# Optimization experiments

Hardware: AMD Instinct MI355X
Metric: run time of the kernel (lower is better)

The kernel has to match this reference:

```python
import jax, jax.numpy as jnp
import numpy as np

TEMPERATURE = 0.2
HYPER_GAMMA = 0.5
EPS = 1e-12  # torch F.normalize / cosine_similarity eps guard (1e-12 / 1e-8)

def setup_inputs() -> dict:
    key = jax.random.key(0)
    k1, k2 = jax.random.split(key)
    B, D = 4096, 1024
    return {
        "emb_i": jax.random.normal(k1, (B, D), dtype=jnp.float32),
        "emb_j": jax.random.normal(k2, (B, D), dtype=jnp.float32),
    }

def _l2_normalize(x, eps=EPS):
    n = jnp.sqrt(jnp.sum(x * x, axis=1, keepdims=True))
    return x / jnp.maximum(n, eps)

def reference(emb_i, emb_j):
    B = emb_i.shape[0]
    z_i = _l2_normalize(emb_i)
    z_j = _l2_normalize(emb_j)
    # cosine similarity of unit vectors == dot product; sim[a, b] = <z_j[a], z_i[b]>
    sim = jnp.einsum('ad,bd->ab', z_j, z_i)  # [B, B]
    sim_positive = jnp.diagonal(sim)
    positives_exp = jnp.exp(-sim_positive + TEMPERATURE)
    neg_mask = 1.0 - jnp.eye(B, dtype=sim.dtype)
    negatives_exp = neg_mask * jnp.exp(sim - TEMPERATURE)
    positives_sum = jnp.sum(jnp.log1p(positives_exp)) / B
    negatives_sum = jnp.sum(jnp.log1p(negatives_exp)) / (B * (B - 1))
    return HYPER_GAMMA * positives_sum + (1.0 - HYPER_GAMMA) * negatives_sum
```

## Files before the change

### kernel.cpp

```cpp
#include <hip/hip_runtime.h>
#include <math.h>

#define B_ROWS 4096
#define D_DIM  1024
static constexpr float TEMP = 0.2f;

typedef __attribute__((ext_vector_type(8))) short bf16x8;
typedef __attribute__((ext_vector_type(4))) float f32x4;

__device__ inline unsigned short f2bf(float f) {
    unsigned int u = __float_as_uint(f);
    u += 0x7fffu + ((u >> 16) & 1u);
    return (unsigned short)(u >> 16);
}

__device__ inline void gload_lds16(const unsigned short* g, unsigned short* l) {
    __builtin_amdgcn_global_load_lds(
        (const __attribute__((address_space(1))) unsigned int*)g,
        (__attribute__((address_space(3))) unsigned int*)l,
        16, 0, 0);
}


__global__ __launch_bounds__(256) void norm_cast_kernel(
        const float* __restrict__ emb_i, const float* __restrict__ emb_j,
        unsigned short* __restrict__ Zi, unsigned short* __restrict__ Zj,
        float* __restrict__ w) {
    const int tid = threadIdx.x;
    if (blockIdx.x == 0 && tid == 0) {
        w[0] = 0.0f; w[1] = 0.0f;
        ((unsigned int*)w)[2] = 0u;
    }
    const int wave = tid >> 6, lane = tid & 63;
    const int row = blockIdx.x * 4 + wave;
    const float* src; unsigned short* dst; int r;
    if (row < B_ROWS) { src = emb_i; dst = Zi; r = row; }
    else              { src = emb_j; dst = Zj; r = row - B_ROWS; }

    const float4* p = (const float4*)(src + (size_t)r * D_DIM);
    float4 v0 = p[lane], v1 = p[64 + lane], v2 = p[128 + lane], v3 = p[192 + lane];
    float s = v0.x*v0.x + v0.y*v0.y + v0.z*v0.z + v0.w*v0.w
            + v1.x*v1.x + v1.y*v1.y + v1.z*v1.z + v1.w*v1.w
            + v2.x*v2.x + v2.y*v2.y + v2.z*v2.z + v2.w*v2.w
            + v3.x*v3.x + v3.y*v3.y + v3.z*v3.z + v3.w*v3.w;
    #pragma unroll
    for (int m = 1; m < 64; m <<= 1) s += __shfl_xor(s, m, 64);
    const float inv = 1.0f / fmaxf(sqrtf(s), 1e-12f);

    ushort4* q = (ushort4*)(dst + (size_t)r * D_DIM);
    ushort4 o0 = { f2bf(v0.x*inv), f2bf(v0.y*inv), f2bf(v0.z*inv), f2bf(v0.w*inv) };
    ushort4 o1 = { f2bf(v1.x*inv), f2bf(v1.y*inv), f2bf(v1.z*inv), f2bf(v1.w*inv) };
    ushort4 o2 = { f2bf(v2.x*inv), f2bf(v2.y*inv), f2bf(v2.z*inv), f2bf(v2.w*inv) };
    ushort4 o3 = { f2bf(v3.x*inv), f2bf(v3.y*inv), f2bf(v3.z*inv), f2bf(v3.w*inv) };
    q[lane] = o0; q[64 + lane] = o1; q[128 + lane] = o2; q[192 + lane] = o3;
}

__global__ __launch_bounds__(256, 2) void simloss_mfma_kernel(
        const unsigned short* __restrict__ Zi,
        const unsigned short* __restrict__ Zj,
        float* __restrict__ w, float* __restrict__ out) {
    __shared__ __align__(16) unsigned short lA[128 * 32];
    __shared__ __align__(16) unsigned short lB[256 * 32];
    __shared__ float rn[4], rp[4];

    const int tid  = threadIdx.x;
    const int lane = tid & 63;
    const int wave = tid >> 6;
    const int wy = wave >> 1, wx = wave & 1;
    const int rowBase = blockIdx.y * 128;
    const int colBase = blockIdx.x * 256;

    const int lrow = lane >> 2;
    const int lp   = lane & 3;
    const int lc   = (lp - (lrow >> 1)) & 3;
    const unsigned short* gA0 = Zj + (size_t)(rowBase + (2*wave+0)*16 + lrow) * D_DIM + lc*8;
    const unsigned short* gA1 = Zj + (size_t)(rowBase + (2*wave+1)*16 + lrow) * D_DIM + lc*8;
    const unsigned short* gB0 = Zi + (size_t)(colBase + (4*wave+0)*16 + lrow) * D_DIM + lc*8;
    const unsigned short* gB1 = Zi + (size_t)(colBase + (4*wave+1)*16 + lrow) * D_DIM + lc*8;
    const unsigned short* gB2 = Zi + (size_t)(colBase + (4*wave+2)*16 + lrow) * D_DIM + lc*8;
    const unsigned short* gB3 = Zi + (size_t)(colBase + (4*wave+3)*16 + lrow) * D_DIM + lc*8;
    unsigned short* sA0 = lA + (2*wave+0) * 512;
    unsigned short* sA1 = lA + (2*wave+1) * 512;
    unsigned short* sB0 = lB + (4*wave+0) * 512;
    unsigned short* sB1 = lB + (4*wave+1) * 512;
    unsigned short* sB2 = lB + (4*wave+2) * 512;
    unsigned short* sB3 = lB + (4*wave+3) * 512;

    const int fr = lane & 15;
    const int q4 = lane >> 4;
    const int p0 = (q4 + (fr >> 1)) & 3;
    const unsigned short* fA = lA + (wy * 64 + fr) * 32 + p0 * 8;
    const unsigned short* fB = lB + (wx * 128 + fr) * 32 + p0 * 8;

    f32x4 acc[4][8];
    #pragma unroll
    for (int i = 0; i < 4; ++i)
        #pragma unroll
        for (int j = 0; j < 8; ++j)
            acc[i][j] = (f32x4){0.f, 0.f, 0.f, 0.f};

    for (int k0 = 0; k0 < D_DIM; k0 += 32) {
        __syncthreads();
        gload_lds16(gA0, sA0); gload_lds16(gA1, sA1);
        gload_lds16(gB0, sB0); gload_lds16(gB1, sB1);
        gload_lds16(gB2, sB2); gload_lds16(gB3, sB3);
        gA0 += 32; gA1 += 32; gB0 += 32; gB1 += 32; gB2 += 32; gB3 += 32;
        __syncthreads();

        bf16x8 a[4], b[8];
        #pragma unroll
        for (int i = 0; i < 4; ++i) a[i] = *(const bf16x8*)(fA + i * 16 * 32);
        #pragma unroll
        for (int j = 0; j < 8; ++j) b[j] = *(const bf16x8*)(fB + j * 16 * 32);
        #pragma unroll
        for (int i = 0; i < 4; ++i)
            #pragma unroll
            for (int j = 0; j < 8; ++j)
                acc[i][j] = __builtin_amdgcn_mfma_f32_16x16x32_bf16(
                    a[i], b[j], acc[i][j], 0, 0, 0);
    }

    const int cr = q4 * 4;
    const int cc = lane & 15;
    float neg = 0.f, pos = 0.f;
    #pragma unroll
    for (int i = 0; i < 4; ++i) {
        const int abase = rowBase + wy * 64 + i * 16 + cr;
        #pragma unroll
        for (int j = 0; j < 8; ++j) {
            const int b = colBase + wx * 128 + j * 16 + cc;
            #pragma unroll
            for (int r = 0; r < 4; ++r) {
                const float x = acc[i][j][r] - TEMP;
                if (abase + r == b) pos += __logf(1.0f + __expf(-x));
                else                neg += __logf(1.0f + __expf(x));
            }
        }
    }
    #pragma unroll
    for (int off = 32; off > 0; off >>= 1) {
        neg += __shfl_down(neg, off, 64);
        pos += __shfl_down(pos, off, 64);
    }
    if (lane == 0) { rn[wave] = neg; rp[wave] = pos; }
    __syncthreads();
    if (tid == 0) {
        atomicAdd(&w[1], rn[0] + rn[1] + rn[2] + rn[3]);
        if ((int)blockIdx.x == (int)(blockIdx.y >> 1))
            atomicAdd(&w[0], rp[0] + rp[1] + rp[2] + rp[3]);
        __threadfence();
        unsigned int done = atomicAdd(((unsigned int*)w) + 2, 1u);
        if (done == gridDim.x * gridDim.y - 1) {
            const float psum = atomicAdd(&w[0], 0.0f);
            const float nsum = atomicAdd(&w[1], 0.0f);
            out[0] = 0.5f * (psum / (float)B_ROWS)
                   + 0.5f * (nsum / ((float)B_ROWS * (float)(B_ROWS - 1)));
        }
    }
}

extern "C" void kernel_launch(void* const* d_in, const int* in_sizes, int n_in,
                              void* d_out, int out_size, void* d_ws, size_t ws_size,
                              hipStream_t stream) {
    const float* emb_i = (const float*)d_in[0];
    const float* emb_j = (const float*)d_in[1];
    float* w = (float*)d_ws;
    unsigned short* Zi = (unsigned short*)(w + 16);
    unsigned short* Zj = Zi + (size_t)B_ROWS * D_DIM;
    float* out = (float*)d_out;

    norm_cast_kernel<<<2 * B_ROWS / 4, 256, 0, stream>>>(emb_i, emb_j, Zi, Zj, w);
    dim3 grid(B_ROWS / 256, B_ROWS / 128);
    simloss_mfma_kernel<<<grid, 256, 0, stream>>>(Zi, Zj, w, out);
}
```

Baseline: 125.9 us.

## Fuse normalize-cast into GEMM kernel with grid-wide spin barrier

```diff
diff --git a/kernel.cpp b/kernel.cpp
--- a/kernel.cpp
+++ b/kernel.cpp
@@ -22,43 +22,15 @@
 }
 
 
-__global__ __launch_bounds__(256) void norm_cast_kernel(
-        const float* __restrict__ emb_i, const float* __restrict__ emb_j,
-        unsigned short* __restrict__ Zi, unsigned short* __restrict__ Zj,
-        float* __restrict__ w) {
-    const int tid = threadIdx.x;
-    if (blockIdx.x == 0 && tid == 0) {
-        w[0] = 0.0f; w[1] = 0.0f;
-        ((unsigned int*)w)[2] = 0u;
-    }
-    const int wave = tid >> 6, lane = tid & 63;
-    const int row = blockIdx.x * 4 + wave;
-    const float* src; unsigned short* dst; int r;
-    if (row < B_ROWS) { src = emb_i; dst = Zi; r = row; }
-    else              { src = emb_j; dst = Zj; r = row - B_ROWS; }
-
-    const float4* p = (const float4*)(src + (size_t)r * D_DIM);
-    float4 v0 = p[lane], v1 = p[64 + lane], v2 = p[128 + lane], v3 = p[192 + lane];
-    float s = v0.x*v0.x + v0.y*v0.y + v0.z*v0.z + v0.w*v0.w
-            + v1.x*v1.x + v1.y*v1.y + v1.z*v1.z + v1.w*v1.w
-            + v2.x*v2.x + v2.y*v2.y + v2.z*v2.z + v2.w*v2.w
-            + v3.x*v3.x + v3.y*v3.y + v3.z*v3.z + v3.w*v3.w;
-    #pragma unroll
-    for (int m = 1; m < 64; m <<= 1) s += __shfl_xor(s, m, 64);
-    const float inv = 1.0f / fmaxf(sqrtf(s), 1e-12f);
-
-    ushort4* q = (ushort4*)(dst + (size_t)r * D_DIM);
-    ushort4 o0 = { f2bf(v0.x*inv), f2bf(v0.y*inv), f2bf(v0.z*inv), f2bf(v0.w*inv) };
-    ushort4 o1 = { f2bf(v1.x*inv), f2bf(v1.y*inv), f2bf(v1.z*inv), f2bf(v1.w*inv) };
-    ushort4 o2 = { f2bf(v2.x*inv), f2bf(v2.y*inv), f2bf(v2.z*inv), f2bf(v2.w*inv) };
-    ushort4 o3 = { f2bf(v3.x*inv), f2bf(v3.y*inv), f2bf(v3.z*inv), f2bf(v3.w*inv) };
-    q[lane] = o0; q[64 + lane] = o1; q[128 + lane] = o2; q[192 + lane] = o3;
+__global__ void init_ctrl_kernel(float* __restrict__ w) {
+    if (threadIdx.x < 2) w[threadIdx.x] = 0.0f;
+    else if (threadIdx.x < 4) ((unsigned int*)w)[threadIdx.x] = 0u;
 }
 
-__global__ __launch_bounds__(256, 2) void simloss_mfma_kernel(
-        const unsigned short* __restrict__ Zi,
-        const unsigned short* __restrict__ Zj,
-        float* __restrict__ w, float* __restrict__ out) {
+__global__ __launch_bounds__(256, 2) void fused_simloss_kernel(
+        const float* __restrict__ emb_i, const float* __restrict__ emb_j,
+        unsigned short* Zi, unsigned short* Zj,
+        float* w, float* out) {
     __shared__ __align__(16) unsigned short lA[128 * 32];
     __shared__ __align__(16) unsigned short lB[256 * 32];
     __shared__ float rn[4], rp[4];
@@ -66,6 +38,45 @@
     const int tid  = threadIdx.x;
     const int lane = tid & 63;
     const int wave = tid >> 6;
+    const int bid  = blockIdx.y * gridDim.x + blockIdx.x;
+    const unsigned int nblk = gridDim.x * gridDim.y;
+
+    #pragma unroll
+    for (int it = 0; it < 4; ++it) {
+        const int row = bid * 16 + it * 4 + wave;
+        const float* src; unsigned short* dst; int r;
+        if (row < B_ROWS) { src = emb_i; dst = Zi; r = row; }
+        else              { src = emb_j; dst = Zj; r = row - B_ROWS; }
+
+        const float4* p = (const float4*)(src + (size_t)r * D_DIM);
+        float4 v0 = p[lane], v1 = p[64 + lane], v2 = p[128 + lane], v3 = p[192 + lane];
+        float s = v0.x*v0.x + v0.y*v0.y + v0.z*v0.z + v0.w*v0.w
+                + v1.x*v1.x + v1.y*v1.y + v1.z*v1.z + v1.w*v1.w
+                + v2.x*v2.x + v2.y*v2.y + v2.z*v2.z + v2.w*v2.w
+                + v3.x*v3.x + v3.y*v3.y + v3.z*v3.z + v3.w*v3.w;
+        #pragma unroll
+        for (int m = 1; m < 64; m <<= 1) s += __shfl_xor(s, m, 64);
+        const float inv = 1.0f / fmaxf(sqrtf(s), 1e-12f);
+
+        ushort4* q = (ushort4*)(dst + (size_t)r * D_DIM);
+        ushort4 o0 = { f2bf(v0.x*inv), f2bf(v0.y*inv), f2bf(v0.z*inv), f2bf(v0.w*inv) };
+        ushort4 o1 = { f2bf(v1.x*inv), f2bf(v1.y*inv), f2bf(v1.z*inv), f2bf(v1.w*inv) };
+        ushort4 o2 = { f2bf(v2.x*inv), f2bf(v2.y*inv), f2bf(v2.z*inv), f2bf(v2.w*inv) };
+        ushort4 o3 = { f2bf(v3.x*inv), f2bf(v3.y*inv), f2bf(v3.z*inv), f2bf(v3.w*inv) };
+        q[lane] = o0; q[64 + lane] = o1; q[128 + lane] = o2; q[192 + lane] = o3;
+    }
+
+    __syncthreads();
+    unsigned int* ctr = (unsigned int*)w + 2;
+    if (tid == 0) {
+        __threadfence();
+        __hip_atomic_fetch_add(ctr, 1u, __ATOMIC_RELEASE, __HIP_MEMORY_SCOPE_AGENT);
+        while (__hip_atomic_load(ctr, __ATOMIC_ACQUIRE, __HIP_MEMORY_SCOPE_AGENT) < nblk)
+            __builtin_amdgcn_s_sleep(8);
+        __threadfence();
+    }
+    __syncthreads();
+
     const int wy = wave >> 1, wx = wave & 1;
     const int rowBase = blockIdx.y * 128;
     const int colBase = blockIdx.x * 256;
@@ -149,8 +160,8 @@
         if ((int)blockIdx.x == (int)(blockIdx.y >> 1))
             atomicAdd(&w[0], rp[0] + rp[1] + rp[2] + rp[3]);
         __threadfence();
-        unsigned int done = atomicAdd(((unsigned int*)w) + 2, 1u);
-        if (done == gridDim.x * gridDim.y - 1) {
+        unsigned int done = atomicAdd(((unsigned int*)w) + 3, 1u);
+        if (done == nblk - 1) {
             const float psum = atomicAdd(&w[0], 0.0f);
             const float nsum = atomicAdd(&w[1], 0.0f);
             out[0] = 0.5f * (psum / (float)B_ROWS)
@@ -169,7 +180,7 @@
     unsigned short* Zj = Zi + (size_t)B_ROWS * D_DIM;
     float* out = (float*)d_out;
 
-    norm_cast_kernel<<<2 * B_ROWS / 4, 256, 0, stream>>>(emb_i, emb_j, Zi, Zj, w);
+    init_ctrl_kernel<<<1, 64, 0, stream>>>(w);
     dim3 grid(B_ROWS / 256, B_ROWS / 128);
-    simloss_mfma_kernel<<<grid, 256, 0, stream>>>(Zi, Zj, w, out);
+    fused_simloss_kernel<<<grid, 256, 0, stream>>>(emb_i, emb_j, Zi, Zj, w, out);
 }
```

Measured after the change: 195.7 us. +55.5%, slower.

## Switch similarity GEMM from bf16 to scaled fp8 e4m3 MFMA

Applied to the files above, without the earlier changes.

```diff
diff --git a/kernel.cpp b/kernel.cpp
--- a/kernel.cpp
+++ b/kernel.cpp
@@ -4,17 +4,39 @@
 #define B_ROWS 4096
 #define D_DIM  1024
 static constexpr float TEMP = 0.2f;
-
-typedef __attribute__((ext_vector_type(8))) short bf16x8;
+static constexpr float FP8_SCALE = 16.0f;
+static constexpr float INV_S2 = 1.0f / 256.0f;
+
 typedef __attribute__((ext_vector_type(4))) float f32x4;
 
-__device__ inline unsigned short f2bf(float f) {
+__device__ inline unsigned char f2fp8(float f) {
     unsigned int u = __float_as_uint(f);
-    u += 0x7fffu + ((u >> 16) & 1u);
-    return (unsigned short)(u >> 16);
-}
-
-__device__ inline void gload_lds16(const unsigned short* g, unsigned short* l) {
+    unsigned int s = (u >> 24) & 0x80u;
+    float af = fabsf(f);
+    unsigned char b;
+    if (af >= 0x1.0p-6f) {
+        unsigned int au = u & 0x7fffffffu;
+        unsigned int lsb = (au >> 20) & 1u;
+        au += 0x7ffffu + lsb;
+        int e = (int)(au >> 23) - 127 + 7;
+        unsigned int m = (au >> 20) & 7u;
+        if (e > 15 || (e == 15 && m > 6)) b = 0x7e;
+        else b = (unsigned char)((e << 3) | m);
+    } else {
+        int q = (int)rintf(af * 512.0f);
+        b = (unsigned char)(q >= 8 ? 0x08 : q);
+    }
+    return (unsigned char)(b | s);
+}
+
+__device__ inline unsigned int f2fp8x4(float4 v) {
+    return (unsigned int)f2fp8(v.x)
+         | ((unsigned int)f2fp8(v.y) << 8)
+         | ((unsigned int)f2fp8(v.z) << 16)
+         | ((unsigned int)f2fp8(v.w) << 24);
+}
+
+__device__ inline void gload_lds16(const unsigned char* g, unsigned char* l) {
     __builtin_amdgcn_global_load_lds(
         (const __attribute__((address_space(1))) unsigned int*)g,
         (__attribute__((address_space(3))) unsigned int*)l,
@@ -24,7 +46,7 @@
 
 __global__ __launch_bounds__(256) void norm_cast_kernel(
         const float* __restrict__ emb_i, const float* __restrict__ emb_j,
-        unsigned short* __restrict__ Zi, unsigned short* __restrict__ Zj,
+        unsigned char* __restrict__ Zi8, unsigned char* __restrict__ Zj8,
         float* __restrict__ w) {
     const int tid = threadIdx.x;
     if (blockIdx.x == 0 && tid == 0) {
@@ -33,9 +55,9 @@
     }
     const int wave = tid >> 6, lane = tid & 63;
     const int row = blockIdx.x * 4 + wave;
-    const float* src; unsigned short* dst; int r;
-    if (row < B_ROWS) { src = emb_i; dst = Zi; r = row; }
-    else              { src = emb_j; dst = Zj; r = row - B_ROWS; }
+    const float* src; unsigned char* dst; int r;
+    if (row < B_ROWS) { src = emb_i; dst = Zi8; r = row; }
+    else              { src = emb_j; dst = Zj8; r = row - B_ROWS; }
 
     const float4* p = (const float4*)(src + (size_t)r * D_DIM);
     float4 v0 = p[lane], v1 = p[64 + lane], v2 = p[128 + lane], v3 = p[192 + lane];
@@ -45,22 +67,25 @@
             + v3.x*v3.x + v3.y*v3.y + v3.z*v3.z + v3.w*v3.w;
     #pragma unroll
     for (int m = 1; m < 64; m <<= 1) s += __shfl_xor(s, m, 64);
-    const float inv = 1.0f / fmaxf(sqrtf(s), 1e-12f);
-
-    ushort4* q = (ushort4*)(dst + (size_t)r * D_DIM);
-    ushort4 o0 = { f2bf(v0.x*inv), f2bf(v0.y*inv), f2bf(v0.z*inv), f2bf(v0.w*inv) };
-    ushort4 o1 = { f2bf(v1.x*inv), f2bf(v1.y*inv), f2bf(v1.z*inv), f2bf(v1.w*inv) };
-    ushort4 o2 = { f2bf(v2.x*inv), f2bf(v2.y*inv), f2bf(v2.z*inv), f2bf(v2.w*inv) };
-    ushort4 o3 = { f2bf(v3.x*inv), f2bf(v3.y*inv), f2bf(v3.z*inv), f2bf(v3.w*inv) };
-    q[lane] = o0; q[64 + lane] = o1; q[128 + lane] = o2; q[192 + lane] = o3;
-}
-
-__global__ __launch_bounds__(256, 2) void simloss_mfma_kernel(
-        const unsigned short* __restrict__ Zi,
-        const unsigned short* __restrict__ Zj,
+    const float inv = FP8_SCALE / fmaxf(sqrtf(s), 1e-12f);
+
+    float4 a0 = {v0.x*inv, v0.y*inv, v0.z*inv, v0.w*inv};
+    float4 a1 = {v1.x*inv, v1.y*inv, v1.z*inv, v1.w*inv};
+    float4 a2 = {v2.x*inv, v2.y*inv, v2.z*inv, v2.w*inv};
+    float4 a3 = {v3.x*inv, v3.y*inv, v3.z*inv, v3.w*inv};
+    unsigned int* q = (unsigned int*)(dst + (size_t)r * D_DIM);
+    q[lane]       = f2fp8x4(a0);
+    q[64 + lane]  = f2fp8x4(a1);
+    q[128 + lane] = f2fp8x4(a2);
+    q[192 + lane] = f2fp8x4(a3);
+}
+
+__global__ __launch_bounds__(256, 2) void simloss_mfma_fp8_kernel(
+        const unsigned char* __restrict__ Zi8,
+        const unsigned char* __restrict__ Zj8,
         float* __restrict__ w, float* __restrict__ out) {
-    __shared__ __align__(16) unsigned short lA[128 * 32];
-    __shared__ __align__(16) unsigned short lB[256 * 32];
+    __shared__ __align__(16) unsigned char lA[128 * 64];
+    __shared__ __align__(16) unsigned char lB[256 * 64];
     __shared__ float rn[4], rp[4];
 
     const int tid  = threadIdx.x;
@@ -72,25 +97,29 @@
 
     const int lrow = lane >> 2;
     const int lp   = lane & 3;
-    const int lc   = (lp - (lrow >> 1)) & 3;
-    const unsigned short* gA0 = Zj + (size_t)(rowBase + (2*wave+0)*16 + lrow) * D_DIM + lc*8;
-    const unsigned short* gA1 = Zj + (size_t)(rowBase + (2*wave+1)*16 + lrow) * D_DIM + lc*8;
-    const unsigned short* gB0 = Zi + (size_t)(colBase + (4*wave+0)*16 + lrow) * D_DIM + lc*8;
-    const unsigned short* gB1 = Zi + (size_t)(colBase + (4*wave+1)*16 + lrow) * D_DIM + lc*8;
-    const unsigned short* gB2 = Zi + (size_t)(colBase + (4*wave+2)*16 + lrow) * D_DIM + lc*8;
-    const unsigned short* gB3 = Zi + (size_t)(colBase + (4*wave+3)*16 + lrow) * D_DIM + lc*8;
-    unsigned short* sA0 = lA + (2*wave+0) * 512;
-    unsigned short* sA1 = lA + (2*wave+1) * 512;
-    unsigned short* sB0 = lB + (4*wave+0) * 512;
-    unsigned short* sB1 = lB + (4*wave+1) * 512;
-    unsigned short* sB2 = lB + (4*wave+2) * 512;
-    unsigned short* sB3 = lB + (4*wave+3) * 512;
+    const int lc   = (lp - (lrow >> 2)) & 3;
+    const unsigned char* gA0 = Zj8 + (size_t)(rowBase + (2*wave+0)*16 + lrow) * D_DIM + lc*16;
+    const unsigned char* gA1 = Zj8 + (size_t)(rowBase + (2*wave+1)*16 + lrow) * D_DIM + lc*16;
+    const unsigned char* gB0 = Zi8 + (size_t)(colBase + (4*wave+0)*16 + lrow) * D_DIM + lc*16;
+    const unsigned char* gB1 = Zi8 + (size_t)(colBase + (4*wave+1)*16 + lrow) * D_DIM + lc*16;
+    const unsigned char* gB2 = Zi8 + (size_t)(colBase + (4*wave+2)*16 + lrow) * D_DIM + lc*16;
+    const unsigned char* gB3 = Zi8 + (size_t)(colBase + (4*wave+3)*16 + lrow) * D_DIM + lc*16;
+    unsigned char* sA0 = lA + (2*wave+0) * 1024;
+    unsigned char* sA1 = lA + (2*wave+1) * 1024;
+    unsigned char* sB0 = lB + (4*wave+0) * 1024;
+    unsigned char* sB1 = lB + (4*wave+1) * 1024;
+    unsigned char* sB2 = lB + (4*wave+2) * 1024;
+    unsigned char* sB3 = lB + (4*wave+3) * 1024;
 
     const int fr = lane & 15;
     const int q4 = lane >> 4;
-    const int p0 = (q4 + (fr >> 1)) & 3;
-    const unsigned short* fA = lA + (wy * 64 + fr) * 32 + p0 * 8;
-    const unsigned short* fB = lB + (wx * 128 + fr) * 32 + p0 * 8;
+    const int qh = q4 >> 1, qb = q4 & 1;
+    const int P0 = (qh + 0 + (fr >> 2)) & 3;
+    const int P1 = (qh + 2 + (fr >> 2)) & 3;
+    const unsigned char* fA0 = lA + (wy * 64 + fr) * 64 + P0 * 16 + qb * 8;
+    const unsigned char* fA1 = lA + (wy * 64 + fr) * 64 + P1 * 16 + qb * 8;
+    const unsigned char* fB0 = lB + (wx * 128 + fr) * 64 + P0 * 16 + qb * 8;
+    const unsigned char* fB1 = lB + (wx * 128 + fr) * 64 + P1 * 16 + qb * 8;
 
     f32x4 acc[4][8];
     #pragma unroll
@@ -99,25 +128,40 @@
         for (int j = 0; j < 8; ++j)
             acc[i][j] = (f32x4){0.f, 0.f, 0.f, 0.f};
 
-    for (int k0 = 0; k0 < D_DIM; k0 += 32) {
+    for (int k0 = 0; k0 < D_DIM; k0 += 64) {
         __syncthreads();
         gload_lds16(gA0, sA0); gload_lds16(gA1, sA1);
         gload_lds16(gB0, sB0); gload_lds16(gB1, sB1);
         gload_lds16(gB2, sB2); gload_lds16(gB3, sB3);
-        gA0 += 32; gA1 += 32; gB0 += 32; gB1 += 32; gB2 += 32; gB3 += 32;
+        gA0 += 64; gA1 += 64; gB0 += 64; gB1 += 64; gB2 += 64; gB3 += 64;
         __syncthreads();
 
-        bf16x8 a[4], b[8];
-        #pragma unroll
-        for (int i = 0; i < 4; ++i) a[i] = *(const bf16x8*)(fA + i * 16 * 32);
-        #pragma unroll
-        for (int j = 0; j < 8; ++j) b[j] = *(const bf16x8*)(fB + j * 16 * 32);
-        #pragma unroll
-        for (int i = 0; i < 4; ++i)
-            #pragma unroll
-            for (int j = 0; j < 8; ++j)
-                acc[i][j] = __builtin_amdgcn_mfma_f32_16x16x32_bf16(
-                    a[i], b[j], acc[i][j], 0, 0, 0);
+        {
+            long a[4], b[8];
+            #pragma unroll
+            for (int i = 0; i < 4; ++i) a[i] = *(const long*)(fA0 + i * 1024);
+            #pragma unroll
+            for (int j = 0; j < 8; ++j) b[j] = *(const long*)(fB0 + j * 1024);
+            #pragma unroll
+            for (int i = 0; i < 4; ++i)
+                #pragma unroll
+                for (int j = 0; j < 8; ++j)
+                    acc[i][j] = __builtin_amdgcn_mfma_f32_16x16x32_fp8_fp8(
+                        a[i], b[j], acc[i][j], 0, 0, 0);
+        }
+        {
+            long a[4], b[8];
+            #pragma unroll
+            for (int i = 0; i < 4; ++i) a[i] = *(const long*)(fA1 + i * 1024);
+            #pragma unroll
+            for (int j = 0; j < 8; ++j) b[j] = *(const long*)(fB1 + j * 1024);
+            #pragma unroll
+            for (int i = 0; i < 4; ++i)
+                #pragma unroll
+                for (int j = 0; j < 8; ++j)
+                    acc[i][j] = __builtin_amdgcn_mfma_f32_16x16x32_fp8_fp8(
+                        a[i], b[j], acc[i][j], 0, 0, 0);
+        }
     }
 
     const int cr = q4 * 4;
@@ -131,7 +175,7 @@
             const int b = colBase + wx * 128 + j * 16 + cc;
             #pragma unroll
             for (int r = 0; r < 4; ++r) {
-                const float x = acc[i][j][r] - TEMP;
+                const float x = acc[i][j][r] * INV_S2 - TEMP;
                 if (abase + r == b) pos += __logf(1.0f + __expf(-x));
                 else                neg += __logf(1.0f + __expf(x));
             }
@@ -165,11 +209,11 @@
     const float* emb_i = (const float*)d_in[0];
     const float* emb_j = (const float*)d_in[1];
     float* w = (float*)d_ws;
-    unsigned short* Zi = (unsigned short*)(w + 16);
-    unsigned short* Zj = Zi + (size_t)B_ROWS * D_DIM;
+    unsigned char* Zi8 = (unsigned char*)(w + 16);
+    unsigned char* Zj8 = Zi8 + (size_t)B_ROWS * D_DIM;
     float* out = (float*)d_out;
 
-    norm_cast_kernel<<<2 * B_ROWS / 4, 256, 0, stream>>>(emb_i, emb_j, Zi, Zj, w);
+    norm_cast_kernel<<<2 * B_ROWS / 4, 256, 0, stream>>>(emb_i, emb_j, Zi8, Zj8, w);
     dim3 grid(B_ROWS / 256, B_ROWS / 128);
-    simloss_mfma_kernel<<<grid, 256, 0, stream>>>(Zi, Zj, w, out);
-}
+    simloss_mfma_fp8_kernel<<<grid, 256, 0, stream>>>(Zi8, Zj8, w, out);
+}
```

Result: faster. 117.9 us (-6.3%).
